# Kernel tuning notes

Measured on AMD Instinct MI355X. Metric: run time of the kernel, lower is better.

The kernel has to match this reference:

```python
import jax, jax.numpy as jnp
import numpy as np

B, S, D, F, T, NS, L, H = 8, 1024, 1024, 4096, 64, 512, 32, 16
TAG_RATE = 0.5      # config.tagging_rate
GSR = 0.5           # config.gate_scaling_rate
ATT_EPS = 1e-12     # config.layer_norm_eps (att_norm)
ENC_EPS = 1e-5      # torch TransformerEncoderLayer default


def _ln(x, g, b, eps):
    m = x.mean(-1, keepdims=True)
    v = x.var(-1, keepdims=True)
    return (x - m) * jax.lax.rsqrt(v + eps) * g + b


def _rope(x):
    # standard rotary embedding over the full hidden dim
    d = x.shape[-1]
    s = x.shape[1]
    inv = 1.0 / (10000.0 ** (jnp.arange(0, d, 2, dtype=jnp.float32) / d))
    ang = jnp.arange(s, dtype=jnp.float32)[:, None] * inv[None, :]  # [S, D/2]
    sin, cos = jnp.sin(ang), jnp.cos(ang)
    x1, x2 = x[..., 0::2], x[..., 1::2]
    return jnp.stack([x1 * cos - x2 * sin, x1 * sin + x2 * cos], axis=-1).reshape(x.shape)


def setup_inputs() -> dict:
    key = jax.random.key(0)
    ks = jax.random.split(key, 24)
    p = lambda k, shp: (0.02 * jax.random.normal(k, shp, dtype=jnp.float32))
    inp = {
        'word_embedding': jax.random.normal(ks[0], (B, S, D), dtype=jnp.float32),
        'attention_mask': jnp.ones((B, S), dtype=jnp.int32),
        'span_batch': jax.random.randint(ks[1], (NS,), 0, B, dtype=jnp.int32),
        'span_start': jax.random.randint(ks[2], (NS,), 0, S - L, dtype=jnp.int32),
        'span_tag': jax.random.randint(ks[3], (NS,), 0, T, dtype=jnp.int32),
        'tag_emb': p(ks[4], (T, D)),
        'gate_w': p(ks[5], (D, 1)),
        'gate_b': jnp.zeros((1,), jnp.float32),
        'attn_ln_g': jnp.ones((D,), jnp.float32),
        'attn_ln_b': jnp.zeros((D,), jnp.float32),
        'in_proj_w': p(ks[6], (3 * D, D)),
        'in_proj_b': jnp.zeros((3 * D,), jnp.float32),
        'out_proj_w': p(ks[7], (D, D)),
        'out_proj_b': jnp.zeros((D,), jnp.float32),
        'enc_ln1_g': jnp.ones((D,), jnp.float32),
        'enc_ln1_b': jnp.zeros((D,), jnp.float32),
        'lin1_w': p(ks[8], (F, D)),
        'lin1_b': jnp.zeros((F,), jnp.float32),
        'lin2_w': p(ks[9], (D, F)),
        'lin2_b': jnp.zeros((D,), jnp.float32),
        'enc_ln2_g': jnp.ones((D,), jnp.float32),
        'enc_ln2_b': jnp.zeros((D,), jnp.float32),
    }
    return inp


def _mha(x, pad, in_proj_w, in_proj_b, out_proj_w, out_proj_b):
    b, s, d = x.shape
    hd = d // H
    qkv = x @ in_proj_w.T + in_proj_b                       # [B,S,3D]
    q, k, v = jnp.split(qkv, 3, axis=-1)
    rs = lambda t: t.reshape(b, s, H, hd).transpose(0, 2, 1, 3)  # [B,H,S,hd]
    q, k, v = rs(q), rs(k), rs(v)
    scores = jnp.einsum('bhqd,bhkd->bhqk', q, k) / jnp.sqrt(jnp.float32(hd))
    scores = jnp.where(pad[:, None, None, :], jnp.float32(-1e30), scores)
    attn = jax.nn.softmax(scores, axis=-1)
    o = jnp.einsum('bhqk,bhkd->bhqd', attn, v).transpose(0, 2, 1, 3).reshape(b, s, d)
    return o @ out_proj_w.T + out_proj_b


def reference(word_embedding, attention_mask, span_batch, span_start, span_tag,
              tag_emb, gate_w, gate_b, attn_ln_g, attn_ln_b,
              in_proj_w, in_proj_b, out_proj_w, out_proj_b,
              enc_ln1_g, enc_ln1_b, lin1_w, lin1_b, lin2_w, lin2_b,
              enc_ln2_g, enc_ln2_b):
    raw = word_embedding                        # dropout off (eval)
    we = _rope(word_embedding)
    # ragged gather -> gate -> scatter-add over fixed-length spans
    tok = span_start[:, None] + jnp.arange(L, dtype=jnp.int32)[None, :]  # [NS,L]
    X = we[span_batch[:, None], tok]            # [NS,L,D]
    gate = GSR * jax.nn.sigmoid(X @ gate_w + gate_b) + (1.0 - GSR) / 2.0  # [NS,L,1]
    res = gate * tag_emb[span_tag][:, None, :] * jnp.float32(L)          # [NS,L,D]
    taged = jnp.zeros_like(word_embedding).at[span_batch[:, None], tok].add(res)
    out_emb = raw + taged * TAG_RATE            # if_merge_by_add
    out_emb = _ln(out_emb, attn_ln_g, attn_ln_b, ATT_EPS)
    pad = attention_mask == 0
    # torch TransformerEncoderLayer (post-norm, relu)
    a = _mha(out_emb, pad, in_proj_w, in_proj_b, out_proj_w, out_proj_b)
    x = _ln(out_emb + a, enc_ln1_g, enc_ln1_b, ENC_EPS)
    ff = jax.nn.relu(x @ lin1_w.T + lin1_b) @ lin2_w.T + lin2_b
    enc = _ln(x + ff, enc_ln2_g, enc_ln2_b, ENC_EPS)
    return enc + out_emb
```

## Files before the change

kernel.cpp:

```cpp
#include <hip/hip_runtime.h>

#define DEV __device__ __forceinline__

typedef short bf16x8 __attribute__((ext_vector_type(8)));
typedef float f32x4 __attribute__((ext_vector_type(4)));
typedef unsigned short u16;
typedef unsigned int u32;

typedef __attribute__((address_space(3))) void lds_void;
typedef __attribute__((address_space(1))) void gbl_void;

DEV void async_copy16(void* lds_dst, const void* g_src) {
    __builtin_amdgcn_global_load_lds((gbl_void*)g_src, (lds_void*)lds_dst, 16, 0, 0);
}

DEV u16 f2bf(float x) {
    u32 u = __float_as_uint(x);
    return (u16)((u + 0x7fffu + ((u >> 16) & 1u)) >> 16);
}
DEV u16 f2bf_fast(float x) {
    return (u16)((__float_as_uint(x) + 0x8000u) >> 16);
}
DEV float bf2f(u16 v) { return __uint_as_float(((u32)v) << 16); }

__global__ __launch_bounds__(256) void f2bf_kernel(const float* __restrict__ src,
                                                   u16* __restrict__ dst, int n4) {
    const int i = blockIdx.x * 256 + threadIdx.x;
    if (i < n4) {
        const float4 v = ((const float4*)src)[i];
        ushort4 o;
        o.x = f2bf(v.x); o.y = f2bf(v.y); o.z = f2bf(v.z); o.w = f2bf(v.w);
        ((ushort4*)dst)[i] = o;
    }
}

#define SPAN_CAP 64

__global__ __launch_bounds__(256) void zero_kernel(int* __restrict__ p, int n) {
    const int i = blockIdx.x * 256 + threadIdx.x;
    if (i < n) p[i] = 0;
}

__global__ void rowlist_kernel(const int* __restrict__ sb,
                               const int* __restrict__ ss,
                               const int* __restrict__ stg,
                               int* __restrict__ cnt, u16* __restrict__ tags) {
    const int n = blockIdx.x;
    const int l = threadIdx.x;
    const int row = sb[n] * 1024 + ss[n] + l;
    const int idx = atomicAdd(&cnt[row], 1);
    if (idx < SPAN_CAP) tags[row * SPAN_CAP + idx] = (u16)stg[n];
}

__global__ __launch_bounds__(256) void lnspan_kernel(
    const float* __restrict__ we, const int* __restrict__ cnt,
    const u16* __restrict__ tags, const float* __restrict__ tag_emb,
    const float* __restrict__ gate_w, const float* __restrict__ gate_b,
    const float* __restrict__ g, const float* __restrict__ bta,
    u16* __restrict__ oe_bf) {
    __shared__ float red[8];
    const int row = blockIdx.x;
    const int s = row & 1023;
    const int t = threadIdx.x;
    float4 x = ((const float4*)(we + (long)row * 1024))[t];

    const float4 gw = ((const float4*)gate_w)[t];
    float dot;
    {
        const float p0 = (float)(2 * t);
        const float p1 = (float)(2 * t + 1);
        const float inv0 = exp2f(p0 * (-13.287712379549449f / 512.0f));
        const float inv1 = exp2f(p1 * (-13.287712379549449f / 512.0f));
        const float a0 = (float)s * inv0, a1 = (float)s * inv1;
        const float s0 = sinf(a0), c0 = cosf(a0);
        const float s1 = sinf(a1), c1 = cosf(a1);
        const float r1a = x.x * c0 - x.y * s0, r2a = x.x * s0 + x.y * c0;
        const float r1b = x.z * c1 - x.w * s1, r2b = x.z * s1 + x.w * c1;
        dot = r1a * gw.x + r2a * gw.y + r1b * gw.z + r2b * gw.w;
    }
#pragma unroll
    for (int off = 32; off > 0; off >>= 1) dot += __shfl_xor(dot, off, 64);
    if ((t & 63) == 0) red[t >> 6] = dot;
    __syncthreads();
    const float z = red[0] + red[1] + red[2] + red[3] + gate_b[0];
    const float gate = 0.25f + 0.5f / (1.f + __expf(-z));
    const float coef = gate * 16.f;

    const int c = min(cnt[row], SPAN_CAP);
    float4 add = {0.f, 0.f, 0.f, 0.f};
    for (int k = 0; k < c; ++k) {
        const int tag = tags[row * SPAN_CAP + k];
        const float4 te = ((const float4*)(tag_emb + (long)tag * 1024))[t];
        add.x += te.x; add.y += te.y; add.z += te.z; add.w += te.w;
    }
    x.x += coef * add.x; x.y += coef * add.y;
    x.z += coef * add.z; x.w += coef * add.w;

    __syncthreads();
    float sm = x.x + x.y + x.z + x.w;
#pragma unroll
    for (int off = 32; off > 0; off >>= 1) sm += __shfl_xor(sm, off, 64);
    if ((t & 63) == 0) red[t >> 6] = sm;
    __syncthreads();
    const float mean = (red[0] + red[1] + red[2] + red[3]) * (1.f / 1024.f);
    float4 dx;
    dx.x = x.x - mean; dx.y = x.y - mean; dx.z = x.z - mean; dx.w = x.w - mean;
    float ss = dx.x * dx.x + dx.y * dx.y + dx.z * dx.z + dx.w * dx.w;
#pragma unroll
    for (int off = 32; off > 0; off >>= 1) ss += __shfl_xor(ss, off, 64);
    if ((t & 63) == 0) red[4 + (t >> 6)] = ss;
    __syncthreads();
    const float var = (red[4] + red[5] + red[6] + red[7]) * (1.f / 1024.f);
    const float rstd = rsqrtf(var + 1e-12f);
    const float4 gv = ((const float4*)g)[t];
    const float4 bv = ((const float4*)bta)[t];
    ushort4 o;
    o.x = f2bf(dx.x * rstd * gv.x + bv.x);
    o.y = f2bf(dx.y * rstd * gv.y + bv.y);
    o.z = f2bf(dx.z * rstd * gv.z + bv.z);
    o.w = f2bf(dx.w * rstd * gv.w + bv.w);
    ((ushort4*)(oe_bf + (long)row * 1024))[t] = o;
}

template <bool WRITE_F32, bool WRITE_BF, bool FINAL>
__global__ __launch_bounds__(256) void ln_kernel(
    const float* __restrict__ X, const float* __restrict__ g,
    const float* __restrict__ bta, float eps, float* __restrict__ Yf,
    u16* __restrict__ Ybf, const u16* __restrict__ addend) {
    __shared__ float red[8];
    const long row = blockIdx.x;
    const int t = threadIdx.x;
    const float4 x = ((const float4*)(X + row * 1024))[t];
    float s = x.x + x.y + x.z + x.w;
#pragma unroll
    for (int off = 32; off > 0; off >>= 1) s += __shfl_xor(s, off, 64);
    if ((t & 63) == 0) red[t >> 6] = s;
    __syncthreads();
    const float mean = (red[0] + red[1] + red[2] + red[3]) * (1.f / 1024.f);
    float4 dx;
    dx.x = x.x - mean; dx.y = x.y - mean; dx.z = x.z - mean; dx.w = x.w - mean;
    float ss = dx.x * dx.x + dx.y * dx.y + dx.z * dx.z + dx.w * dx.w;
#pragma unroll
    for (int off = 32; off > 0; off >>= 1) ss += __shfl_xor(ss, off, 64);
    if ((t & 63) == 0) red[4 + (t >> 6)] = ss;
    __syncthreads();
    const float var = (red[4] + red[5] + red[6] + red[7]) * (1.f / 1024.f);
    const float rstd = rsqrtf(var + eps);
    const float4 gv = ((const float4*)g)[t];
    const float4 bv = ((const float4*)bta)[t];
    float4 y;
    y.x = dx.x * rstd * gv.x + bv.x;
    y.y = dx.y * rstd * gv.y + bv.y;
    y.z = dx.z * rstd * gv.z + bv.z;
    y.w = dx.w * rstd * gv.w + bv.w;
    if (FINAL) {
        const ushort4 a = ((const ushort4*)(addend + row * 1024))[t];
        y.x += bf2f(a.x); y.y += bf2f(a.y); y.z += bf2f(a.z); y.w += bf2f(a.w);
    }
    if (WRITE_F32) ((float4*)(Yf + row * 1024))[t] = y;
    if (WRITE_BF) {
        ushort4 o;
        o.x = f2bf(y.x); o.y = f2bf(y.y); o.z = f2bf(y.z); o.w = f2bf(y.w);
        ((ushort4*)(Ybf + row * 1024))[t] = o;
    }
}

template <bool OUT_BF16, bool RELU, bool HAS_RES>
__global__ __launch_bounds__(256, 2) void gemm_nt(
    const u16* __restrict__ A, const u16* __restrict__ B,
    const float* __restrict__ bias, const u16* __restrict__ res,
    void* __restrict__ Cout, int N, int K) {
    __shared__ u16 Al[8192];
    __shared__ u16 Bl[8192];
    const int tid = threadIdx.x;
    const int wave = tid >> 6;
    const int lane = tid & 63;
    const int quad = lane >> 4;
    const int lq = lane & 15;
    const int wm = wave >> 1;
    const int wn = wave & 1;
    const long rowBase = (long)blockIdx.x * 128;
    const long colBase = (long)blockIdx.y * 128;

    f32x4 acc[4][4];
    const f32x4 fzero = {0.f, 0.f, 0.f, 0.f};
#pragma unroll
    for (int i = 0; i < 4; ++i)
#pragma unroll
        for (int j = 0; j < 4; ++j) acc[i][j] = fzero;

    const int rX = tid >> 3;
    const int pX = (tid & 7) ^ (rX & 7);
    const u16* gA = A + (rowBase + rX) * (long)K + pX * 8;
    const u16* gB = B + (colBase + rX) * (long)K + pX * 8;
    u16* ldsA = Al + wave * 512;
    u16* ldsB = Bl + wave * 512;

    for (int kt = 0; kt < K; kt += 64) {
        __syncthreads();
#pragma unroll
        for (int c = 0; c < 4; ++c) {
            async_copy16(ldsA + c * 2048, gA + (long)c * 32 * K + kt);
            async_copy16(ldsB + c * 2048, gB + (long)c * 32 * K + kt);
        }
        __syncthreads();
#pragma unroll
        for (int ks = 0; ks < 2; ++ks) {
            bf16x8 af[4], bfr[4];
#pragma unroll
            for (int i = 0; i < 4; ++i) {
                const int r = wm * 64 + i * 16 + lq;
                af[i] = *(const bf16x8*)&Al[r * 64 + (((ks * 4 + quad) ^ (lq & 7)) * 8)];
            }
#pragma unroll
            for (int j = 0; j < 4; ++j) {
                const int r = wn * 64 + j * 16 + lq;
                bfr[j] = *(const bf16x8*)&Bl[r * 64 + (((ks * 4 + quad) ^ (lq & 7)) * 8)];
            }
#pragma unroll
            for (int i = 0; i < 4; ++i)
#pragma unroll
                for (int j = 0; j < 4; ++j)
                    acc[i][j] = __builtin_amdgcn_mfma_f32_16x16x32_bf16(
                        af[i], bfr[j], acc[i][j], 0, 0, 0);
        }
    }

    float biasv[4];
#pragma unroll
    for (int j = 0; j < 4; ++j) biasv[j] = bias[colBase + wn * 64 + j * 16 + lq];
#pragma unroll
    for (int i = 0; i < 4; ++i) {
        const long grow = rowBase + wm * 64 + i * 16 + quad * 4;
#pragma unroll
        for (int j = 0; j < 4; ++j) {
            const long gcol = colBase + wn * 64 + j * 16 + lq;
#pragma unroll
            for (int r = 0; r < 4; ++r) {
                float v = acc[i][j][r] + biasv[j];
                if (RELU) v = fmaxf(v, 0.f);
                if (HAS_RES) v += bf2f(res[(grow + r) * N + gcol]);
                if (OUT_BF16)
                    ((u16*)Cout)[(grow + r) * N + gcol] = f2bf(v);
                else
                    ((float*)Cout)[(grow + r) * N + gcol] = v;
            }
        }
    }
}

__global__ __launch_bounds__(256) void vtrans_kernel(const u16* __restrict__ QKV,
                                                     u16* __restrict__ Vt) {
    __shared__ u16 tile[64][72];
    const int bid = blockIdx.x;
    const int st = bid & 15;
    const int h = (bid >> 4) & 15;
    const int b = bid >> 8;
    const int t = threadIdx.x;
    const int sl = t >> 2;
    const int dc = (t & 3) * 16;
    const u16* src = QKV + ((long)(b * 1024 + st * 64 + sl)) * 3072 + 2048 + h * 64 + dc;
    *(uint4*)&tile[sl][dc] = *(const uint4*)src;
    *(uint4*)&tile[sl][dc + 8] = *(const uint4*)(src + 8);
    __syncthreads();
    const int dl = t >> 2;
    const int sc = (t & 3) * 16;
    union { u16 u[16]; uint4 q[2]; } tmp;
#pragma unroll
    for (int i = 0; i < 16; ++i) tmp.u[i] = tile[sc + i][dl];
    u16* dst = Vt + ((long)(b * 16 + h) * 64 + dl) * 1024 + st * 64 + sc;
    *(uint4*)dst = tmp.q[0];
    *(uint4*)(dst + 8) = tmp.q[1];
}

__global__ __launch_bounds__(256, 4) void attn_kernel(
    const u16* __restrict__ QKV, const u16* __restrict__ Vt,
    const int* __restrict__ mask, u16* __restrict__ Out) {
    __shared__ u16 KL[4096];
    __shared__ u16 VL[4096];
    __shared__ u16 PL[4][16 * 72];
    const int tid = threadIdx.x;
    const int wid = tid >> 6;
    const int lane = tid & 63;
    const int quad = lane >> 4;
    const int lq = lane & 15;
    const int slot0 = quad ^ (lq & 7);
    const int slot1 = slot0 ^ 4;

    const int bid = blockIdx.x;
    const int qb = bid & 7;
    const int h = (bid >> 3) & 15;
    const int b = bid >> 7;
    const int qbase = qb * 128 + wid * 32;

    bf16x8 aq[2][2];
#pragma unroll
    for (int t = 0; t < 2; ++t) {
        const u16* qp = QKV + ((long)(b * 1024 + qbase + t * 16 + lq)) * 3072 +
                        h * 64 + quad * 8;
        aq[t][0] = *(const bf16x8*)qp;
        aq[t][1] = *(const bf16x8*)(qp + 32);
    }

    const int c0 = tid, c1 = 256 + tid;
    const int r0 = c0 >> 3, j0 = (c0 & 7) ^ (r0 & 7);
    const int r1 = c1 >> 3, j1 = (c1 & 7) ^ (r1 & 7);
    const u16* srcK0 = QKV + ((long)(b * 1024 + r0)) * 3072 + 1024 + h * 64 + j0 * 8;
    const u16* srcK1 = QKV + ((long)(b * 1024 + r1)) * 3072 + 1024 + h * 64 + j1 * 8;
    const u16* srcV0 = Vt + ((long)(b * 16 + h) * 64 + r0) * 1024 + j0 * 8;
    const u16* srcV1 = Vt + ((long)(b * 16 + h) * 64 + r1) * 1024 + j1 * 8;
    u16* ldsK0 = KL + wid * 512;
    u16* ldsK1 = KL + 2048 + wid * 512;
    u16* ldsV0 = VL + wid * 512;
    u16* ldsV1 = VL + 2048 + wid * 512;

    const f32x4 fzero = {0.f, 0.f, 0.f, 0.f};
    f32x4 acc[2][4];
#pragma unroll
    for (int t = 0; t < 2; ++t)
#pragma unroll
        for (int j = 0; j < 4; ++j) acc[t][j] = fzero;
    float lsum[2][4] = {{0.f, 0.f, 0.f, 0.f}, {0.f, 0.f, 0.f, 0.f}};
    u16* myP = PL[wid];
    const int* mrow = mask + b * 1024;

    for (int kt = 0; kt < 1024; kt += 64) {
        __syncthreads();
        async_copy16(ldsK0, srcK0 + (long)kt * 3072);
        async_copy16(ldsK1, srcK1 + (long)kt * 3072);
        async_copy16(ldsV0, srcV0 + kt);
        async_copy16(ldsV1, srcV1 + kt);
        __syncthreads();

        bf16x8 kf0[4], kf1[4];
#pragma unroll
        for (int ct = 0; ct < 4; ++ct) {
            const int rowb = (ct * 16 + lq) * 64;
            kf0[ct] = *(const bf16x8*)&KL[rowb + slot0 * 8];
            kf1[ct] = *(const bf16x8*)&KL[rowb + slot1 * 8];
        }
        float mw[4];
#pragma unroll
        for (int ct = 0; ct < 4; ++ct) mw[ct] = mrow[kt + ct * 16 + lq] ? 1.f : 0.f;

#pragma unroll
        for (int t = 0; t < 2; ++t) {
            f32x4 s[4];
#pragma unroll
            for (int ct = 0; ct < 4; ++ct) {
                s[ct] = __builtin_amdgcn_mfma_f32_16x16x32_bf16(aq[t][0], kf0[ct],
                                                                fzero, 0, 0, 0);
                s[ct] = __builtin_amdgcn_mfma_f32_16x16x32_bf16(aq[t][1], kf1[ct],
                                                                s[ct], 0, 0, 0);
            }
            asm volatile("s_waitcnt lgkmcnt(0)" ::: "memory");
#pragma unroll
            for (int ct = 0; ct < 4; ++ct)
#pragma unroll
                for (int r = 0; r < 4; ++r) {
                    const float p = mw[ct] * __expf(s[ct][r] * 0.125f);
                    lsum[t][r] += p;
                    myP[(quad * 4 + r) * 72 + ct * 16 + lq] = f2bf_fast(p);
                }
            asm volatile("s_waitcnt lgkmcnt(0)" ::: "memory");
            const bf16x8 pf0 = *(const bf16x8*)&myP[lq * 72 + quad * 8];
            const bf16x8 pf1 = *(const bf16x8*)&myP[lq * 72 + 32 + quad * 8];
#pragma unroll
            for (int j = 0; j < 4; ++j) {
                const int rowb = (j * 16 + lq) * 64;
                const bf16x8 vf0 = *(const bf16x8*)&VL[rowb + slot0 * 8];
                const bf16x8 vf1 = *(const bf16x8*)&VL[rowb + slot1 * 8];
                acc[t][j] = __builtin_amdgcn_mfma_f32_16x16x32_bf16(pf0, vf0,
                                                                    acc[t][j], 0, 0, 0);
                acc[t][j] = __builtin_amdgcn_mfma_f32_16x16x32_bf16(pf1, vf1,
                                                                    acc[t][j], 0, 0, 0);
            }
        }
    }

#pragma unroll
    for (int t = 0; t < 2; ++t) {
        float inv[4];
#pragma unroll
        for (int r = 0; r < 4; ++r) {
            float l = lsum[t][r];
#pragma unroll
            for (int off = 1; off < 16; off <<= 1) l += __shfl_xor(l, off, 16);
            inv[r] = 1.f / l;
        }
        const long orow = (long)b * 1024 + qbase + t * 16 + quad * 4;
#pragma unroll
        for (int j = 0; j < 4; ++j)
#pragma unroll
            for (int r = 0; r < 4; ++r)
                Out[(orow + r) * 1024 + h * 64 + j * 16 + lq] =
                    f2bf_fast(acc[t][j][r] * inv[r]);
    }
}

extern "C" void kernel_launch(void* const* d_in, const int* in_sizes, int n_in,
                              void* d_out, int out_size, void* d_ws, size_t ws_size,
                              hipStream_t stream) {
    const float* we        = (const float*)d_in[0];
    const int*   amask     = (const int*)d_in[1];
    const int*   span_b    = (const int*)d_in[2];
    const int*   span_s    = (const int*)d_in[3];
    const int*   span_t    = (const int*)d_in[4];
    const float* tag_emb   = (const float*)d_in[5];
    const float* gate_w    = (const float*)d_in[6];
    const float* gate_b    = (const float*)d_in[7];
    const float* attn_ln_g = (const float*)d_in[8];
    const float* attn_ln_b = (const float*)d_in[9];
    const float* in_proj_w = (const float*)d_in[10];
    const float* in_proj_b = (const float*)d_in[11];
    const float* out_proj_w= (const float*)d_in[12];
    const float* out_proj_b= (const float*)d_in[13];
    const float* enc1_g    = (const float*)d_in[14];
    const float* enc1_b    = (const float*)d_in[15];
    const float* lin1_w    = (const float*)d_in[16];
    const float* lin1_b    = (const float*)d_in[17];
    const float* lin2_w    = (const float*)d_in[18];
    const float* lin2_b    = (const float*)d_in[19];
    const float* enc2_g    = (const float*)d_in[20];
    const float* enc2_b    = (const float*)d_in[21];
    float* out = (float*)d_out;

    char* ws = (char*)d_ws;
    size_t off = 0;
    auto alloc = [&](size_t bytes) {
        void* p = ws + off;
        off += (bytes + 255) & ~(size_t)255;
        return p;
    };
    const size_t MT = 8192;
    u16* oe_bf   = (u16*)alloc(MT * 1024 * 2);
    u16* ax_bf   = (u16*)alloc(MT * 1024 * 2);
    char* region = (char*)alloc((size_t)67108864);
    u16* qkv_bf  = (u16*)region;
    u16* vt_bf   = (u16*)(region + (size_t)MT * 3072 * 2);
    u16* ff1_bf  = (u16*)region;
    u16* wb_inproj  = (u16*)alloc((size_t)3072 * 1024 * 2);
    u16* wb_outproj = (u16*)alloc((size_t)1024 * 1024 * 2);
    u16* wb_lin1    = (u16*)alloc((size_t)4096 * 1024 * 2);
    u16* wb_lin2    = (u16*)alloc((size_t)1024 * 4096 * 2);
    int* row_cnt    = (int*)alloc((size_t)8192 * 4);
    u16* row_tags   = (u16*)alloc((size_t)8192 * SPAN_CAP * 2);

    zero_kernel<<<32, 256, 0, stream>>>(row_cnt, 8192);
    rowlist_kernel<<<512, 32, 0, stream>>>(span_b, span_s, span_t, row_cnt, row_tags);
    f2bf_kernel<<<3072, 256, 0, stream>>>(in_proj_w, wb_inproj, 3072 * 1024 / 4);
    f2bf_kernel<<<1024, 256, 0, stream>>>(out_proj_w, wb_outproj, 1024 * 1024 / 4);
    f2bf_kernel<<<4096, 256, 0, stream>>>(lin1_w, wb_lin1, 4096 * 1024 / 4);
    f2bf_kernel<<<4096, 256, 0, stream>>>(lin2_w, wb_lin2, 1024 * 4096 / 4);
    lnspan_kernel<<<8192, 256, 0, stream>>>(we, row_cnt, row_tags, tag_emb,
                                            gate_w, gate_b, attn_ln_g, attn_ln_b,
                                            oe_bf);
    dim3 g1(64, 24);
    gemm_nt<true, false, false><<<g1, 256, 0, stream>>>(oe_bf, wb_inproj, in_proj_b,
                                                        nullptr, qkv_bf, 3072, 1024);
    vtrans_kernel<<<2048, 256, 0, stream>>>(qkv_bf, vt_bf);
    attn_kernel<<<1024, 256, 0, stream>>>(qkv_bf, vt_bf, amask, ax_bf);
    dim3 g2(64, 8);
    gemm_nt<false, false, true><<<g2, 256, 0, stream>>>(ax_bf, wb_outproj, out_proj_b,
                                                        oe_bf, out, 1024, 1024);
    ln_kernel<false, true, false><<<8192, 256, 0, stream>>>(
        out, enc1_g, enc1_b, 1e-5f, nullptr, ax_bf, nullptr);
    dim3 g3(64, 32);
    gemm_nt<true, true, false><<<g3, 256, 0, stream>>>(ax_bf, wb_lin1, lin1_b,
                                                       nullptr, ff1_bf, 4096, 1024);
    gemm_nt<false, false, true><<<g2, 256, 0, stream>>>(ff1_bf, wb_lin2, lin2_b,
                                                        ax_bf, out, 1024, 4096);
    ln_kernel<true, false, true><<<8192, 256, 0, stream>>>(
        out, enc2_g, enc2_b, 1e-5f, out, nullptr, oe_bf);
}
```

Measured before the change: 523.4 us.

## Fuse prep kernels, replace span rowlist with ballot scan, fuse V transpose

```diff
diff --git a/kernel.cpp b/kernel.cpp
--- a/kernel.cpp
+++ b/kernel.cpp
@@ -6,6 +6,7 @@
 typedef float f32x4 __attribute__((ext_vector_type(4)));
 typedef unsigned short u16;
 typedef unsigned int u32;
+typedef unsigned long long u64;
 
 typedef __attribute__((address_space(3))) void lds_void;
 typedef __attribute__((address_space(1))) void gbl_void;
@@ -23,47 +24,49 @@
 }
 DEV float bf2f(u16 v) { return __uint_as_float(((u32)v) << 16); }
 
-__global__ __launch_bounds__(256) void f2bf_kernel(const float* __restrict__ src,
-                                                   u16* __restrict__ dst, int n4) {
-    const int i = blockIdx.x * 256 + threadIdx.x;
-    if (i < n4) {
+__global__ __launch_bounds__(256) void prep_kernel(
+    const float* __restrict__ we, const int* __restrict__ sb,
+    const int* __restrict__ ss, const int* __restrict__ stg,
+    const float* __restrict__ tag_emb, const float* __restrict__ gate_w,
+    const float* __restrict__ gate_b, const float* __restrict__ g,
+    const float* __restrict__ bta,
+    const float* __restrict__ w0, const float* __restrict__ w1,
+    const float* __restrict__ w2, const float* __restrict__ w3,
+    u16* __restrict__ oe_bf, u16* __restrict__ o0, u16* __restrict__ o1,
+    u16* __restrict__ o2, u16* __restrict__ o3) {
+    const int blk = blockIdx.x;
+    const int t = threadIdx.x;
+
+    if (blk >= 8192) {
+        int base = blk - 8192;
+        const float* src; u16* dst;
+        if (base < 3072)      { src = w0; dst = o0; }
+        else if (base < 4096) { src = w1; dst = o1; base -= 3072; }
+        else if (base < 8192) { src = w2; dst = o2; base -= 4096; }
+        else                  { src = w3; dst = o3; base -= 8192; }
+        const int i = base * 256 + t;
         const float4 v = ((const float4*)src)[i];
         ushort4 o;
         o.x = f2bf(v.x); o.y = f2bf(v.y); o.z = f2bf(v.z); o.w = f2bf(v.w);
         ((ushort4*)dst)[i] = o;
-    }
-}
-
-#define SPAN_CAP 64
-
-__global__ __launch_bounds__(256) void zero_kernel(int* __restrict__ p, int n) {
-    const int i = blockIdx.x * 256 + threadIdx.x;
-    if (i < n) p[i] = 0;
-}
-
-__global__ void rowlist_kernel(const int* __restrict__ sb,
-                               const int* __restrict__ ss,
-                               const int* __restrict__ stg,
-                               int* __restrict__ cnt, u16* __restrict__ tags) {
-    const int n = blockIdx.x;
-    const int l = threadIdx.x;
-    const int row = sb[n] * 1024 + ss[n] + l;
-    const int idx = atomicAdd(&cnt[row], 1);
-    if (idx < SPAN_CAP) tags[row * SPAN_CAP + idx] = (u16)stg[n];
-}
-
-__global__ __launch_bounds__(256) void lnspan_kernel(
-    const float* __restrict__ we, const int* __restrict__ cnt,
-    const u16* __restrict__ tags, const float* __restrict__ tag_emb,
-    const float* __restrict__ gate_w, const float* __restrict__ gate_b,
-    const float* __restrict__ g, const float* __restrict__ bta,
-    u16* __restrict__ oe_bf) {
+        return;
+    }
+
     __shared__ float red[8];
-    const int row = blockIdx.x;
+    __shared__ u64 smask[8];
+    const int row = blk;
+    const int b = row >> 10;
     const int s = row & 1023;
-    const int t = threadIdx.x;
+
+    {
+        const bool m0 = (sb[t] == b) && ((u32)(s - ss[t]) < 32u);
+        const bool m1 = (sb[t + 256] == b) && ((u32)(s - ss[t + 256]) < 32u);
+        const u64 b0 = __ballot(m0);
+        const u64 b1 = __ballot(m1);
+        if ((t & 63) == 0) { smask[t >> 6] = b0; smask[4 + (t >> 6)] = b1; }
+    }
+
     float4 x = ((const float4*)(we + (long)row * 1024))[t];
-
     const float4 gw = ((const float4*)gate_w)[t];
     float dot;
     {
@@ -86,12 +89,18 @@
     const float gate = 0.25f + 0.5f / (1.f + __expf(-z));
     const float coef = gate * 16.f;
 
-    const int c = min(cnt[row], SPAN_CAP);
     float4 add = {0.f, 0.f, 0.f, 0.f};
-    for (int k = 0; k < c; ++k) {
-        const int tag = tags[row * SPAN_CAP + k];
-        const float4 te = ((const float4*)(tag_emb + (long)tag * 1024))[t];
-        add.x += te.x; add.y += te.y; add.z += te.z; add.w += te.w;
+#pragma unroll
+    for (int gi = 0; gi < 8; ++gi) {
+        u64 m = smask[gi];
+        const int nb = (gi & 3) * 64 + (gi >> 2) * 256;
+        while (m) {
+            const int bit = __ffsll(m) - 1;
+            m &= m - 1;
+            const int tag = stg[nb + bit];
+            const float4 te = ((const float4*)(tag_emb + (long)tag * 1024))[t];
+            add.x += te.x; add.y += te.y; add.z += te.z; add.w += te.w;
+        }
     }
     x.x += coef * add.x; x.y += coef * add.y;
     x.z += coef * add.z; x.w += coef * add.w;
@@ -105,10 +114,10 @@
     const float mean = (red[0] + red[1] + red[2] + red[3]) * (1.f / 1024.f);
     float4 dx;
     dx.x = x.x - mean; dx.y = x.y - mean; dx.z = x.z - mean; dx.w = x.w - mean;
-    float ss = dx.x * dx.x + dx.y * dx.y + dx.z * dx.z + dx.w * dx.w;
-#pragma unroll
-    for (int off = 32; off > 0; off >>= 1) ss += __shfl_xor(ss, off, 64);
-    if ((t & 63) == 0) red[4 + (t >> 6)] = ss;
+    float ss2 = dx.x * dx.x + dx.y * dx.y + dx.z * dx.z + dx.w * dx.w;
+#pragma unroll
+    for (int off = 32; off > 0; off >>= 1) ss2 += __shfl_xor(ss2, off, 64);
+    if ((t & 63) == 0) red[4 + (t >> 6)] = ss2;
     __syncthreads();
     const float var = (red[4] + red[5] + red[6] + red[7]) * (1.f / 1024.f);
     const float rstd = rsqrtf(var + 1e-12f);
@@ -165,11 +174,11 @@
     }
 }
 
-template <bool OUT_BF16, bool RELU, bool HAS_RES>
+template <bool OUT_BF16, bool RELU, bool HAS_RES, bool VTRANS>
 __global__ __launch_bounds__(256, 2) void gemm_nt(
     const u16* __restrict__ A, const u16* __restrict__ B,
     const float* __restrict__ bias, const u16* __restrict__ res,
-    void* __restrict__ Cout, int N, int K) {
+    void* __restrict__ Cout, int N, int K, u16* __restrict__ vt) {
     __shared__ u16 Al[8192];
     __shared__ u16 Bl[8192];
     const int tid = threadIdx.x;
@@ -240,37 +249,21 @@
                 float v = acc[i][j][r] + biasv[j];
                 if (RELU) v = fmaxf(v, 0.f);
                 if (HAS_RES) v += bf2f(res[(grow + r) * N + gcol]);
-                if (OUT_BF16)
+                if (VTRANS && gcol >= 2048) {
+                    const int hh = (int)(gcol - 2048) >> 6;
+                    const int dd = (int)(gcol - 2048) & 63;
+                    const long rr = grow + r;
+                    const int bb = (int)(rr >> 10);
+                    const int sR = (int)(rr & 1023);
+                    vt[(((long)bb * 16 + hh) * 64 + dd) * 1024 + sR] = f2bf(v);
+                } else if (OUT_BF16) {
                     ((u16*)Cout)[(grow + r) * N + gcol] = f2bf(v);
-                else
+                } else {
                     ((float*)Cout)[(grow + r) * N + gcol] = v;
+                }
             }
         }
     }
-}
-
-__global__ __launch_bounds__(256) void vtrans_kernel(const u16* __restrict__ QKV,
-                                                     u16* __restrict__ Vt) {
-    __shared__ u16 tile[64][72];
-    const int bid = blockIdx.x;
-    const int st = bid & 15;
-    const int h = (bid >> 4) & 15;
-    const int b = bid >> 8;
-    const int t = threadIdx.x;
-    const int sl = t >> 2;
-    const int dc = (t & 3) * 16;
-    const u16* src = QKV + ((long)(b * 1024 + st * 64 + sl)) * 3072 + 2048 + h * 64 + dc;
-    *(uint4*)&tile[sl][dc] = *(const uint4*)src;
-    *(uint4*)&tile[sl][dc + 8] = *(const uint4*)(src + 8);
-    __syncthreads();
-    const int dl = t >> 2;
-    const int sc = (t & 3) * 16;
-    union { u16 u[16]; uint4 q[2]; } tmp;
-#pragma unroll
-    for (int i = 0; i < 16; ++i) tmp.u[i] = tile[sc + i][dl];
-    u16* dst = Vt + ((long)(b * 16 + h) * 64 + dl) * 1024 + st * 64 + sc;
-    *(uint4*)dst = tmp.q[0];
-    *(uint4*)(dst + 8) = tmp.q[1];
 }
 
 __global__ __launch_bounds__(256, 4) void attn_kernel(
@@ -443,33 +436,25 @@
     u16* wb_outproj = (u16*)alloc((size_t)1024 * 1024 * 2);
     u16* wb_lin1    = (u16*)alloc((size_t)4096 * 1024 * 2);
     u16* wb_lin2    = (u16*)alloc((size_t)1024 * 4096 * 2);
-    int* row_cnt    = (int*)alloc((size_t)8192 * 4);
-    u16* row_tags   = (u16*)alloc((size_t)8192 * SPAN_CAP * 2);
-
-    zero_kernel<<<32, 256, 0, stream>>>(row_cnt, 8192);
-    rowlist_kernel<<<512, 32, 0, stream>>>(span_b, span_s, span_t, row_cnt, row_tags);
-    f2bf_kernel<<<3072, 256, 0, stream>>>(in_proj_w, wb_inproj, 3072 * 1024 / 4);
-    f2bf_kernel<<<1024, 256, 0, stream>>>(out_proj_w, wb_outproj, 1024 * 1024 / 4);
-    f2bf_kernel<<<4096, 256, 0, stream>>>(lin1_w, wb_lin1, 4096 * 1024 / 4);
-    f2bf_kernel<<<4096, 256, 0, stream>>>(lin2_w, wb_lin2, 1024 * 4096 / 4);
-    lnspan_kernel<<<8192, 256, 0, stream>>>(we, row_cnt, row_tags, tag_emb,
-                                            gate_w, gate_b, attn_ln_g, attn_ln_b,
-                                            oe_bf);
+
+    prep_kernel<<<20480, 256, 0, stream>>>(
+        we, span_b, span_s, span_t, tag_emb, gate_w, gate_b,
+        attn_ln_g, attn_ln_b, in_proj_w, out_proj_w, lin1_w, lin2_w,
+        oe_bf, wb_inproj, wb_outproj, wb_lin1, wb_lin2);
     dim3 g1(64, 24);
-    gemm_nt<true, false, false><<<g1, 256, 0, stream>>>(oe_bf, wb_inproj, in_proj_b,
-                                                        nullptr, qkv_bf, 3072, 1024);
-    vtrans_kernel<<<2048, 256, 0, stream>>>(qkv_bf, vt_bf);
+    gemm_nt<true, false, false, true><<<g1, 256, 0, stream>>>(
+        oe_bf, wb_inproj, in_proj_b, nullptr, qkv_bf, 3072, 1024, vt_bf);
     attn_kernel<<<1024, 256, 0, stream>>>(qkv_bf, vt_bf, amask, ax_bf);
     dim3 g2(64, 8);
-    gemm_nt<false, false, true><<<g2, 256, 0, stream>>>(ax_bf, wb_outproj, out_proj_b,
-                                                        oe_bf, out, 1024, 1024);
+    gemm_nt<false, false, true, false><<<g2, 256, 0, stream>>>(
+        ax_bf, wb_outproj, out_proj_b, oe_bf, out, 1024, 1024, nullptr);
     ln_kernel<false, true, false><<<8192, 256, 0, stream>>>(
         out, enc1_g, enc1_b, 1e-5f, nullptr, ax_bf, nullptr);
     dim3 g3(64, 32);
-    gemm_nt<true, true, false><<<g3, 256, 0, stream>>>(ax_bf, wb_lin1, lin1_b,
-                                                       nullptr, ff1_bf, 4096, 1024);
-    gemm_nt<false, false, true><<<g2, 256, 0, stream>>>(ff1_bf, wb_lin2, lin2_b,
-                                                        ax_bf, out, 1024, 4096);
+    gemm_nt<true, true, false, false><<<g3, 256, 0, stream>>>(
+        ax_bf, wb_lin1, lin1_b, nullptr, ff1_bf, 4096, 1024, nullptr);
+    gemm_nt<false, false, true, false><<<g2, 256, 0, stream>>>(
+        ff1_bf, wb_lin2, lin2_b, ax_bf, out, 1024, 4096, nullptr);
     ln_kernel<true, false, true><<<8192, 256, 0, stream>>>(
         out, enc2_g, enc2_b, 1e-5f, out, nullptr, oe_bf);
 }
```

Measured after the change: 483.8 us, median of 2. 7.6% less time.
